# Kernel tuning notes

Hardware: AMD Instinct MI355X
Metric: run time of the kernel (lower is better)

The kernel has to match this reference:

```python
import jax, jax.numpy as jnp
import numpy as np

U, I, D, NNZ = 100000, 50000, 64, 6000000
N = U + I

def setup_inputs() -> dict:
    key = jax.random.key(0)
    ks = jax.random.split(key, 8)
    return {
        'user_emb': jax.random.normal(ks[0], (U, D), dtype=jnp.float32) * 0.1,
        'item_emb': jax.random.normal(ks[1], (I, D), dtype=jnp.float32) * 0.1,
        'adj_val': jax.random.uniform(ks[2], (NNZ,), dtype=jnp.float32) * 0.01,
        'adj_row': jax.random.randint(ks[3], (NNZ,), 0, N, dtype=jnp.int32),
        'adj_col': jax.random.randint(ks[4], (NNZ,), 0, N, dtype=jnp.int32),
        'users': jax.random.randint(ks[5], (4096,), 0, U, dtype=jnp.int32),
        'pos_items': jax.random.randint(ks[6], (4096,), 0, I, dtype=jnp.int32),
        'neg_items': jax.random.randint(ks[7], (4096,), 0, I, dtype=jnp.int32),
        'num_layers': 3,
    }

def spmm(val, row, col, x, n):
    # out[r] = sum_{e: row[e]==r} val[e] * x[col[e]]
    return jax.ops.segment_sum(val[:, None] * x[col], row, num_segments=n)

def reference(user_emb, item_emb, adj_val, adj_row, adj_col, users, pos_items, neg_items, num_layers):
    n = user_emb.shape[0] + item_emb.shape[0]
    ego = jnp.concatenate([user_emb, item_emb], axis=0)   # [N, D]
    acc = ego
    cur = ego
    for _ in range(num_layers):
        cur = spmm(adj_val, adj_row, adj_col, cur, n)
        acc = acc + cur
    final = acc / jnp.asarray(num_layers + 1, dtype=ego.dtype)  # mean over stacked layers
    u_g = final[:user_emb.shape[0]]
    i_g = final[user_emb.shape[0]:]
    return (u_g[users], i_g[pos_items], i_g[neg_items], u_g, i_g)
```

## Files before the change

kernel.cpp:

```cpp
#include <hip/hip_runtime.h>


#define U_CNT 100000
#define I_CNT 50000
#define N_CNT 150000
#define DIM 64
#define NNZ_CNT 6000000
#define NSEL 4096

#define NBKT 512
#define BROWS 293
#define BKT_OF(r) ((int)(((unsigned long long)(unsigned)(r) * 114521ull) >> 25))
#define BCAP 13312

#define BIN_BLK 512
#define BIN_THR 256

__device__ __forceinline__ unsigned short f32_to_bf16_rne(float f) {
    unsigned u = __float_as_uint(f);
    u += 0x7FFFu + ((u >> 16) & 1u);
    return (unsigned short)(u >> 16);
}
__device__ __forceinline__ float bf16_lo(unsigned u) {
    return __uint_as_float(u << 16);
}
__device__ __forceinline__ float bf16_hi(unsigned u) {
    return __uint_as_float(u & 0xFFFF0000u);
}


__global__ void init_kernel(const float* __restrict__ user_emb,
                            const float* __restrict__ item_emb,
                            unsigned short* __restrict__ cur,
                            float* __restrict__ acc) {
    const int total = N_CNT * DIM / 4;
    const int ubound = U_CNT * DIM / 4;
    const float4* ue = (const float4*)user_emb;
    const float4* ie = (const float4*)item_emb;
    float4* a4 = (float4*)acc;
    ushort4* c4 = (ushort4*)cur;
    for (int i = blockIdx.x * blockDim.x + threadIdx.x; i < total;
         i += gridDim.x * blockDim.x) {
        float4 v = (i < ubound) ? ue[i] : ie[i - ubound];
        ushort4 cv;
        cv.x = f32_to_bf16_rne(v.x);
        cv.y = f32_to_bf16_rne(v.y);
        cv.z = f32_to_bf16_rne(v.z);
        cv.w = f32_to_bf16_rne(v.w);
        c4[i] = cv;
        float4 a = v;
        a.x *= 0.25f; a.y *= 0.25f; a.z *= 0.25f; a.w *= 0.25f;
        a4[i] = a;
    }
}

__global__ void gather_kernel(const float* __restrict__ final_emb,
                              const int* __restrict__ users,
                              const int* __restrict__ pos,
                              const int* __restrict__ neg,
                              float* __restrict__ out) {
    const int total = 3 * NSEL * (DIM / 4);
    const float4* f4 = (const float4*)final_emb;
    float4* o4 = (float4*)out;
    for (int i = blockIdx.x * blockDim.x + threadIdx.x; i < total;
         i += gridDim.x * blockDim.x) {
        const int rowi = i / (DIM / 4);
        const int d4 = i % (DIM / 4);
        int src;
        if (rowi < NSEL) {
            src = users[rowi];
        } else if (rowi < 2 * NSEL) {
            src = U_CNT + pos[rowi - NSEL];
        } else {
            src = U_CNT + neg[rowi - 2 * NSEL];
        }
        o4[i] = f4[src * (DIM / 4) + d4];
    }
}

__global__ void bin_scatter_kernel(const float* __restrict__ val,
                                   const int* __restrict__ row,
                                   const int* __restrict__ col,
                                   int* __restrict__ gcnt,
                                   int2* __restrict__ etmp) {
    __shared__ int h[NBKT];
    __shared__ int curs[NBKT];
    for (int i = threadIdx.x; i < NBKT; i += BIN_THR) h[i] = 0;
    __syncthreads();
    const int tid = blockIdx.x * BIN_THR + threadIdx.x;
    const int4* r4 = (const int4*)row;
    const int4* c4 = (const int4*)col;
    const float4* v4 = (const float4*)val;
    for (int g = tid; g < NNZ_CNT / 4; g += BIN_BLK * BIN_THR) {
        const int4 r = r4[g];
        atomicAdd(&h[BKT_OF(r.x)], 1);
        atomicAdd(&h[BKT_OF(r.y)], 1);
        atomicAdd(&h[BKT_OF(r.z)], 1);
        atomicAdd(&h[BKT_OF(r.w)], 1);
    }
    __syncthreads();
    for (int i = threadIdx.x; i < NBKT; i += BIN_THR) {
        const int c = h[i];
        int base = 0;
        if (c > 0) base = atomicAdd(&gcnt[i], c);
        curs[i] = i * BCAP + base;
    }
    __syncthreads();
    for (int g = tid; g < NNZ_CNT / 4; g += BIN_BLK * BIN_THR) {
        const int4 r = r4[g];
        const int4 c = c4[g];
        const float4 v = v4[g];
        {
            const int bk = BKT_OF(r.x);
            const int p = atomicAdd(&curs[bk], 1);
            etmp[p] = make_int2(c.x | ((r.x - bk * BROWS) << 18),
                                __float_as_int(v.x));
        }
        {
            const int bk = BKT_OF(r.y);
            const int p = atomicAdd(&curs[bk], 1);
            etmp[p] = make_int2(c.y | ((r.y - bk * BROWS) << 18),
                                __float_as_int(v.y));
        }
        {
            const int bk = BKT_OF(r.z);
            const int p = atomicAdd(&curs[bk], 1);
            etmp[p] = make_int2(c.z | ((r.z - bk * BROWS) << 18),
                                __float_as_int(v.z));
        }
        {
            const int bk = BKT_OF(r.w);
            const int p = atomicAdd(&curs[bk], 1);
            etmp[p] = make_int2(c.w | ((r.w - bk * BROWS) << 18),
                                __float_as_int(v.w));
        }
    }
}

__global__ void scan_tot_kernel(const int* __restrict__ gcnt,
                                int* __restrict__ boff) {
    __shared__ int s[NBKT];
    const int k = threadIdx.x;
    const int v = gcnt[k];
    s[k] = v;
    __syncthreads();
    for (int d = 1; d < NBKT; d <<= 1) {
        int t = (k >= d) ? s[k - d] : 0;
        __syncthreads();
        s[k] += t;
        __syncthreads();
    }
    boff[k] = s[k] - v;
    if (k == NBKT - 1) boff[NBKT] = s[k];
}

__global__ __launch_bounds__(1024) void csr_sort_kernel(
        const int2* __restrict__ etmp,
        const int* __restrict__ gcnt,
        const int* __restrict__ boff,
        int2* __restrict__ edges,
        int* __restrict__ off) {
    __shared__ int cnt[BROWS];
    __shared__ int start[BROWS];
    __shared__ int sc[1024];
    const int bkt = blockIdx.x;
    const int n = gcnt[bkt];
    const int sbeg = bkt * BCAP;
    const int dbeg = boff[bkt];
    const int tid = threadIdx.x;

    for (int i = tid; i < BROWS; i += 1024) cnt[i] = 0;
    __syncthreads();
    for (int e = tid; e < n; e += 1024)
        atomicAdd(&cnt[((unsigned)etmp[sbeg + e].x) >> 18], 1);
    __syncthreads();
    {
        const int v = (tid < BROWS) ? cnt[tid] : 0;
        sc[tid] = v;
        __syncthreads();
        for (int d = 1; d < 1024; d <<= 1) {
            int t = (tid >= d) ? sc[tid - d] : 0;
            __syncthreads();
            sc[tid] += t;
            __syncthreads();
        }
        if (tid < BROWS) start[tid] = sc[tid] - v;
    }
    __syncthreads();
    const int base_row = bkt * BROWS;
    for (int i = tid; i < BROWS; i += 1024) {
        if (base_row + i < N_CNT) off[base_row + i] = dbeg + start[i];
        cnt[i] = start[i];
    }
    if (bkt == 0 && tid == 0) off[N_CNT] = NNZ_CNT;
    __syncthreads();
    for (int e = tid; e < n; e += 1024) {
        const int2 ed = etmp[sbeg + e];
        const int rl = ((unsigned)ed.x) >> 18;
        const int p = atomicAdd(&cnt[rl], 1);
        edges[dbeg + p] = make_int2(ed.x & 0x3FFFF, ed.y);
    }
}

__global__ void spmm_csr_kernel(const int2* __restrict__ edges,
                                const int* __restrict__ off,
                                const unsigned short* __restrict__ x,
                                unsigned short* __restrict__ y,
                                float* __restrict__ acc,
                                int write_y) {
    const int lane = threadIdx.x & 63;
    const int o = lane >> 3;
    const int t = lane & 7;
    const int gw = (blockIdx.x * blockDim.x + threadIdx.x) >> 6;
    const int totalWaves = (gridDim.x * blockDim.x) >> 6;
    const unsigned short* xt = x + (t << 3);
    for (int r = gw; r < N_CNT; r += totalWaves) {
        const int beg = off[r];
        const int end = off[r + 1];
        const int nfull = (end - beg) & ~15;
        const int mend = beg + nfull;
        float s0 = 0.f, s1 = 0.f, s2 = 0.f, s3 = 0.f;
        float s4 = 0.f, s5 = 0.f, s6 = 0.f, s7 = 0.f;
        #pragma unroll 2
        for (int e0 = beg; e0 < mend; e0 += 16) {
            const int2 eva = edges[e0 + o];
            const int2 evb = edges[e0 + o + 8];
            const float va = __int_as_float(eva.y);
            const float vb = __int_as_float(evb.y);
            const uint4 xa = *(const uint4*)(xt + ((size_t)(unsigned)eva.x << 6));
            const uint4 xb = *(const uint4*)(xt + ((size_t)(unsigned)evb.x << 6));
            s0 += va * bf16_lo(xa.x); s1 += va * bf16_hi(xa.x);
            s2 += va * bf16_lo(xa.y); s3 += va * bf16_hi(xa.y);
            s4 += va * bf16_lo(xa.z); s5 += va * bf16_hi(xa.z);
            s6 += va * bf16_lo(xa.w); s7 += va * bf16_hi(xa.w);
            s0 += vb * bf16_lo(xb.x); s1 += vb * bf16_hi(xb.x);
            s2 += vb * bf16_lo(xb.y); s3 += vb * bf16_hi(xb.y);
            s4 += vb * bf16_lo(xb.z); s5 += vb * bf16_hi(xb.z);
            s6 += vb * bf16_lo(xb.w); s7 += vb * bf16_hi(xb.w);
        }
        if (mend < end) {
            const int ea = mend + o;
            const int eb = ea + 8;
            int2 eva = make_int2(0, 0), evb = make_int2(0, 0);
            if (ea < end) eva = edges[ea];
            if (eb < end) evb = edges[eb];
            const float va = __int_as_float(eva.y);
            const float vb = __int_as_float(evb.y);
            const uint4 xa = *(const uint4*)(xt + ((size_t)(unsigned)eva.x << 6));
            const uint4 xb = *(const uint4*)(xt + ((size_t)(unsigned)evb.x << 6));
            s0 += va * bf16_lo(xa.x); s1 += va * bf16_hi(xa.x);
            s2 += va * bf16_lo(xa.y); s3 += va * bf16_hi(xa.y);
            s4 += va * bf16_lo(xa.z); s5 += va * bf16_hi(xa.z);
            s6 += va * bf16_lo(xa.w); s7 += va * bf16_hi(xa.w);
            s0 += vb * bf16_lo(xb.x); s1 += vb * bf16_hi(xb.x);
            s2 += vb * bf16_lo(xb.y); s3 += vb * bf16_hi(xb.y);
            s4 += vb * bf16_lo(xb.z); s5 += vb * bf16_hi(xb.z);
            s6 += vb * bf16_lo(xb.w); s7 += vb * bf16_hi(xb.w);
        }
        s0 += __shfl_xor(s0, 8); s0 += __shfl_xor(s0, 16); s0 += __shfl_xor(s0, 32);
        s1 += __shfl_xor(s1, 8); s1 += __shfl_xor(s1, 16); s1 += __shfl_xor(s1, 32);
        s2 += __shfl_xor(s2, 8); s2 += __shfl_xor(s2, 16); s2 += __shfl_xor(s2, 32);
        s3 += __shfl_xor(s3, 8); s3 += __shfl_xor(s3, 16); s3 += __shfl_xor(s3, 32);
        s4 += __shfl_xor(s4, 8); s4 += __shfl_xor(s4, 16); s4 += __shfl_xor(s4, 32);
        s5 += __shfl_xor(s5, 8); s5 += __shfl_xor(s5, 16); s5 += __shfl_xor(s5, 32);
        s6 += __shfl_xor(s6, 8); s6 += __shfl_xor(s6, 16); s6 += __shfl_xor(s6, 32);
        s7 += __shfl_xor(s7, 8); s7 += __shfl_xor(s7, 16); s7 += __shfl_xor(s7, 32);
        if (lane < 8) {
            if (write_y) {
                uint4 cv;
                cv.x = (unsigned)f32_to_bf16_rne(s0) |
                       ((unsigned)f32_to_bf16_rne(s1) << 16);
                cv.y = (unsigned)f32_to_bf16_rne(s2) |
                       ((unsigned)f32_to_bf16_rne(s3) << 16);
                cv.z = (unsigned)f32_to_bf16_rne(s4) |
                       ((unsigned)f32_to_bf16_rne(s5) << 16);
                cv.w = (unsigned)f32_to_bf16_rne(s6) |
                       ((unsigned)f32_to_bf16_rne(s7) << 16);
                ((uint4*)(y + ((size_t)r << 6)))[t] = cv;
            }
            float4* a4 = (float4*)(acc + ((size_t)r << 6) + (t << 3));
            float4 a0 = a4[0];
            float4 a1 = a4[1];
            a0.x += 0.25f * s0; a0.y += 0.25f * s1;
            a0.z += 0.25f * s2; a0.w += 0.25f * s3;
            a1.x += 0.25f * s4; a1.y += 0.25f * s5;
            a1.z += 0.25f * s6; a1.w += 0.25f * s7;
            a4[0] = a0;
            a4[1] = a1;
        }
    }
}


__global__ void init_f32_kernel(const float* __restrict__ user_emb,
                                const float* __restrict__ item_emb,
                                float* __restrict__ cur,
                                float* __restrict__ acc) {
    const int total = N_CNT * DIM / 4;
    const int ubound = U_CNT * DIM / 4;
    const float4* ue = (const float4*)user_emb;
    const float4* ie = (const float4*)item_emb;
    float4* c4 = (float4*)cur;
    float4* a4 = (float4*)acc;
    for (int i = blockIdx.x * blockDim.x + threadIdx.x; i < total;
         i += gridDim.x * blockDim.x) {
        float4 v = (i < ubound) ? ue[i] : ie[i - ubound];
        c4[i] = v;
        float4 a = v;
        a.x *= 0.25f; a.y *= 0.25f; a.z *= 0.25f; a.w *= 0.25f;
        a4[i] = a;
    }
}

__global__ void spmm_atomic_kernel(const float* __restrict__ val,
                                   const int* __restrict__ row,
                                   const int* __restrict__ col,
                                   const float* __restrict__ x,
                                   float* __restrict__ y) {
    const int lane = threadIdx.x & 63;
    const int gw = (blockIdx.x * blockDim.x + threadIdx.x) >> 6;
    const int totalWaves = (gridDim.x * blockDim.x) >> 6;
    for (int base = gw * 64; base < NNZ_CNT; base += totalWaves * 64) {
        const int e = base + lane;
        const float v = val[e];
        const int r = row[e];
        const int c = col[e];
        #pragma unroll 8
        for (int k = 0; k < 64; ++k) {
            const float vk = __shfl(v, k);
            const int rk = __shfl(r, k);
            const int ck = __shfl(c, k);
            atomicAdd(&y[rk * DIM + lane], vk * x[ck * DIM + lane]);
        }
    }
}

__global__ void accum_scale_kernel(float* __restrict__ acc,
                                   const float* __restrict__ nxt,
                                   float wacc) {
    const int total = N_CNT * DIM / 4;
    float4* a4 = (float4*)acc;
    const float4* n4 = (const float4*)nxt;
    for (int i = blockIdx.x * blockDim.x + threadIdx.x; i < total;
         i += gridDim.x * blockDim.x) {
        float4 a = a4[i];
        const float4 n = n4[i];
        a.x += wacc * n.x; a.y += wacc * n.y; a.z += wacc * n.z; a.w += wacc * n.w;
        a4[i] = a;
    }
}


extern "C" void kernel_launch(void* const* d_in, const int* in_sizes, int n_in,
                              void* d_out, int out_size, void* d_ws, size_t ws_size,
                              hipStream_t stream) {
    const float* user_emb  = (const float*)d_in[0];
    const float* item_emb  = (const float*)d_in[1];
    const float* adj_val   = (const float*)d_in[2];
    const int*   adj_row   = (const int*)d_in[3];
    const int*   adj_col   = (const int*)d_in[4];
    const int*   users     = (const int*)d_in[5];
    const int*   pos_items = (const int*)d_in[6];
    const int*   neg_items = (const int*)d_in[7];

    float* out       = (float*)d_out;
    float* out_sel   = out;
    float* final_emb = out + (size_t)3 * NSEL * DIM;
    float* acc       = final_emb;

    const size_t NBH = (size_t)N_CNT * DIM * 2;
    char* ws = (char*)d_ws;
    int2* etmp = (int2*)(ws + 0);
    unsigned short* bufA = (unsigned short*)(ws + 0);
    unsigned short* bufB = (unsigned short*)(ws + NBH);

    const size_t offE    = (size_t)NBKT * BCAP * 8;
    const size_t offG    = offE + (size_t)NNZ_CNT * 8;
    const size_t offBoff = offG + 4096;
    const size_t offOff  = offBoff + 4096;
    const size_t needed  = offOff + (size_t)(N_CNT + 1) * 4 + 64;

    if (ws_size >= needed) {
        int2* edges = (int2*)(ws + offE);
        int*  gcnt  = (int*)(ws + offG);
        int*  boff  = (int*)(ws + offBoff);
        int*  offp  = (int*)(ws + offOff);

        (void)hipMemsetAsync(gcnt, 0, NBKT * sizeof(int), stream);
        bin_scatter_kernel<<<BIN_BLK, BIN_THR, 0, stream>>>(adj_val, adj_row,
                                                            adj_col, gcnt,
                                                            etmp);
        scan_tot_kernel<<<1, NBKT, 0, stream>>>(gcnt, boff);
        csr_sort_kernel<<<NBKT, 1024, 0, stream>>>(etmp, gcnt, boff, edges,
                                                   offp);

        init_kernel<<<2048, 256, 0, stream>>>(user_emb, item_emb, bufA, acc);

        unsigned short* cur = bufA;
        unsigned short* nxt = bufB;
        for (int l = 0; l < 3; ++l) {
            spmm_csr_kernel<<<2048, 256, 0, stream>>>(edges, offp, cur, nxt, acc,
                                                      (l < 2) ? 1 : 0);
            unsigned short* t = cur; cur = nxt; nxt = t;
        }
    } else {
        float* fA = (float*)(ws + 0);
        float* fB = (float*)(ws + (size_t)N_CNT * DIM * sizeof(float));
        init_f32_kernel<<<2048, 256, 0, stream>>>(user_emb, item_emb, fA, acc);
        float* cur = fA;
        float* nxt = fB;
        for (int l = 0; l < 3; ++l) {
            (void)hipMemsetAsync(nxt, 0, (size_t)N_CNT * DIM * sizeof(float),
                                 stream);
            spmm_atomic_kernel<<<2048, 256, 0, stream>>>(adj_val, adj_row,
                                                         adj_col, cur, nxt);
            accum_scale_kernel<<<2048, 256, 0, stream>>>(acc, nxt, 0.25f);
            float* t = cur; cur = nxt; nxt = t;
        }
    }

    gather_kernel<<<768, 256, 0, stream>>>(final_emb, users, pos_items,
                                           neg_items, out_sel);
}
```

Baseline: 466.5 us.

## Fuse bucket-offset scan into CSR sort and interleave two rows per wave in SpMM

Measured after the change: 562.1 us. +20.5%, slower.

```diff
diff --git a/kernel.cpp b/kernel.cpp
--- a/kernel.cpp
+++ b/kernel.cpp
@@ -78,6 +78,7 @@
     }
 }
 
+
 __global__ void bin_scatter_kernel(const float* __restrict__ val,
                                    const int* __restrict__ row,
                                    const int* __restrict__ col,
@@ -137,42 +138,39 @@
     }
 }
 
-__global__ void scan_tot_kernel(const int* __restrict__ gcnt,
-                                int* __restrict__ boff) {
-    __shared__ int s[NBKT];
-    const int k = threadIdx.x;
-    const int v = gcnt[k];
-    s[k] = v;
-    __syncthreads();
-    for (int d = 1; d < NBKT; d <<= 1) {
-        int t = (k >= d) ? s[k - d] : 0;
-        __syncthreads();
-        s[k] += t;
-        __syncthreads();
-    }
-    boff[k] = s[k] - v;
-    if (k == NBKT - 1) boff[NBKT] = s[k];
-}
-
 __global__ __launch_bounds__(1024) void csr_sort_kernel(
         const int2* __restrict__ etmp,
         const int* __restrict__ gcnt,
-        const int* __restrict__ boff,
         int2* __restrict__ edges,
         int* __restrict__ off) {
     __shared__ int cnt[BROWS];
     __shared__ int start[BROWS];
     __shared__ int sc[1024];
     const int bkt = blockIdx.x;
+    const int tid = threadIdx.x;
     const int n = gcnt[bkt];
     const int sbeg = bkt * BCAP;
-    const int dbeg = boff[bkt];
-    const int tid = threadIdx.x;
+
+    sc[tid] = (tid < bkt) ? gcnt[tid] : 0;
+    __syncthreads();
+    for (int d = 512; d >= 1; d >>= 1) {
+        if (tid < d) sc[tid] += sc[tid + d];
+        __syncthreads();
+    }
+    const int dbeg = sc[0];
+    __syncthreads();
 
     for (int i = tid; i < BROWS; i += 1024) cnt[i] = 0;
     __syncthreads();
-    for (int e = tid; e < n; e += 1024)
-        atomicAdd(&cnt[((unsigned)etmp[sbeg + e].x) >> 18], 1);
+    const int npair = n >> 1;
+    const int4* et4 = (const int4*)(etmp + sbeg);
+    for (int p = tid; p < npair; p += 1024) {
+        const int4 ed = et4[p];
+        atomicAdd(&cnt[((unsigned)ed.x) >> 18], 1);
+        atomicAdd(&cnt[((unsigned)ed.z) >> 18], 1);
+    }
+    if (tid == 0 && (n & 1))
+        atomicAdd(&cnt[((unsigned)etmp[sbeg + n - 1].x) >> 18], 1);
     __syncthreads();
     {
         const int v = (tid < BROWS) ? cnt[tid] : 0;
@@ -194,11 +192,100 @@
     }
     if (bkt == 0 && tid == 0) off[N_CNT] = NNZ_CNT;
     __syncthreads();
-    for (int e = tid; e < n; e += 1024) {
-        const int2 ed = etmp[sbeg + e];
+    for (int p = tid; p < npair; p += 1024) {
+        const int4 ed = et4[p];
+        int rl = ((unsigned)ed.x) >> 18;
+        int q = atomicAdd(&cnt[rl], 1);
+        edges[dbeg + q] = make_int2(ed.x & 0x3FFFF, ed.y);
+        rl = ((unsigned)ed.z) >> 18;
+        q = atomicAdd(&cnt[rl], 1);
+        edges[dbeg + q] = make_int2(ed.z & 0x3FFFF, ed.w);
+    }
+    if (tid == 0 && (n & 1)) {
+        const int2 ed = etmp[sbeg + n - 1];
         const int rl = ((unsigned)ed.x) >> 18;
-        const int p = atomicAdd(&cnt[rl], 1);
-        edges[dbeg + p] = make_int2(ed.x & 0x3FFFF, ed.y);
+        const int q = atomicAdd(&cnt[rl], 1);
+        edges[dbeg + q] = make_int2(ed.x & 0x3FFFF, ed.y);
+    }
+}
+
+
+__device__ __forceinline__ void block16(const int2* __restrict__ edges,
+                                        int e0, int o,
+                                        const unsigned short* __restrict__ xt,
+                                        float (&s)[8]) {
+    const int2 eva = edges[e0 + o];
+    const int2 evb = edges[e0 + o + 8];
+    const float va = __int_as_float(eva.y);
+    const float vb = __int_as_float(evb.y);
+    const uint4 xa = *(const uint4*)(xt + ((size_t)(unsigned)eva.x << 6));
+    const uint4 xb = *(const uint4*)(xt + ((size_t)(unsigned)evb.x << 6));
+    s[0] += va * bf16_lo(xa.x); s[1] += va * bf16_hi(xa.x);
+    s[2] += va * bf16_lo(xa.y); s[3] += va * bf16_hi(xa.y);
+    s[4] += va * bf16_lo(xa.z); s[5] += va * bf16_hi(xa.z);
+    s[6] += va * bf16_lo(xa.w); s[7] += va * bf16_hi(xa.w);
+    s[0] += vb * bf16_lo(xb.x); s[1] += vb * bf16_hi(xb.x);
+    s[2] += vb * bf16_lo(xb.y); s[3] += vb * bf16_hi(xb.y);
+    s[4] += vb * bf16_lo(xb.z); s[5] += vb * bf16_hi(xb.z);
+    s[6] += vb * bf16_lo(xb.w); s[7] += vb * bf16_hi(xb.w);
+}
+
+__device__ __forceinline__ void tail16(const int2* __restrict__ edges,
+                                       int mend, int end, int o,
+                                       const unsigned short* __restrict__ xt,
+                                       float (&s)[8]) {
+    const int ea = mend + o;
+    const int eb = ea + 8;
+    int2 eva = make_int2(0, 0), evb = make_int2(0, 0);
+    if (ea < end) eva = edges[ea];
+    if (eb < end) evb = edges[eb];
+    const float va = __int_as_float(eva.y);
+    const float vb = __int_as_float(evb.y);
+    const uint4 xa = *(const uint4*)(xt + ((size_t)(unsigned)eva.x << 6));
+    const uint4 xb = *(const uint4*)(xt + ((size_t)(unsigned)evb.x << 6));
+    s[0] += va * bf16_lo(xa.x); s[1] += va * bf16_hi(xa.x);
+    s[2] += va * bf16_lo(xa.y); s[3] += va * bf16_hi(xa.y);
+    s[4] += va * bf16_lo(xa.z); s[5] += va * bf16_hi(xa.z);
+    s[6] += va * bf16_lo(xa.w); s[7] += va * bf16_hi(xa.w);
+    s[0] += vb * bf16_lo(xb.x); s[1] += vb * bf16_hi(xb.x);
+    s[2] += vb * bf16_lo(xb.y); s[3] += vb * bf16_hi(xb.y);
+    s[4] += vb * bf16_lo(xb.z); s[5] += vb * bf16_hi(xb.z);
+    s[6] += vb * bf16_lo(xb.w); s[7] += vb * bf16_hi(xb.w);
+}
+
+__device__ __forceinline__ void reduce_write(float (&s)[8], int r, int lane,
+                                             int t,
+                                             unsigned short* __restrict__ y,
+                                             float* __restrict__ acc,
+                                             int write_y) {
+    #pragma unroll
+    for (int i = 0; i < 8; ++i) {
+        s[i] += __shfl_xor(s[i], 8);
+        s[i] += __shfl_xor(s[i], 16);
+        s[i] += __shfl_xor(s[i], 32);
+    }
+    if (lane < 8) {
+        if (write_y) {
+            uint4 cv;
+            cv.x = (unsigned)f32_to_bf16_rne(s[0]) |
+                   ((unsigned)f32_to_bf16_rne(s[1]) << 16);
+            cv.y = (unsigned)f32_to_bf16_rne(s[2]) |
+                   ((unsigned)f32_to_bf16_rne(s[3]) << 16);
+            cv.z = (unsigned)f32_to_bf16_rne(s[4]) |
+                   ((unsigned)f32_to_bf16_rne(s[5]) << 16);
+            cv.w = (unsigned)f32_to_bf16_rne(s[6]) |
+                   ((unsigned)f32_to_bf16_rne(s[7]) << 16);
+            ((uint4*)(y + ((size_t)r << 6)))[t] = cv;
+        }
+        float4* a4 = (float4*)(acc + ((size_t)r << 6) + (t << 3));
+        float4 a0 = a4[0];
+        float4 a1 = a4[1];
+        a0.x += 0.25f * s[0]; a0.y += 0.25f * s[1];
+        a0.z += 0.25f * s[2]; a0.w += 0.25f * s[3];
+        a1.x += 0.25f * s[4]; a1.y += 0.25f * s[5];
+        a1.z += 0.25f * s[6]; a1.w += 0.25f * s[7];
+        a4[0] = a0;
+        a4[1] = a1;
     }
 }
 
@@ -214,80 +301,30 @@
     const int gw = (blockIdx.x * blockDim.x + threadIdx.x) >> 6;
     const int totalWaves = (gridDim.x * blockDim.x) >> 6;
     const unsigned short* xt = x + (t << 3);
-    for (int r = gw; r < N_CNT; r += totalWaves) {
-        const int beg = off[r];
-        const int end = off[r + 1];
-        const int nfull = (end - beg) & ~15;
-        const int mend = beg + nfull;
-        float s0 = 0.f, s1 = 0.f, s2 = 0.f, s3 = 0.f;
-        float s4 = 0.f, s5 = 0.f, s6 = 0.f, s7 = 0.f;
+    for (int r0 = gw; r0 < N_CNT; r0 += 2 * totalWaves) {
+        const int r1 = r0 + totalWaves;
+        const int begA = off[r0];
+        const int endA = off[r0 + 1];
+        int begB = 0, endB = 0;
+        if (r1 < N_CNT) { begB = off[r1]; endB = off[r1 + 1]; }
+        const int mendA = begA + ((endA - begA) & ~15);
+        const int mendB = begB + ((endB - begB) & ~15);
+        float sA[8] = {0.f, 0.f, 0.f, 0.f, 0.f, 0.f, 0.f, 0.f};
+        float sB[8] = {0.f, 0.f, 0.f, 0.f, 0.f, 0.f, 0.f, 0.f};
+        int eA = begA, eB = begB;
+        while (eA < mendA && eB < mendB) {
+            block16(edges, eA, o, xt, sA);
+            block16(edges, eB, o, xt, sB);
+            eA += 16; eB += 16;
+        }
         #pragma unroll 2
-        for (int e0 = beg; e0 < mend; e0 += 16) {
-            const int2 eva = edges[e0 + o];
-            const int2 evb = edges[e0 + o + 8];
-            const float va = __int_as_float(eva.y);
-            const float vb = __int_as_float(evb.y);
-            const uint4 xa = *(const uint4*)(xt + ((size_t)(unsigned)eva.x << 6));
-            const uint4 xb = *(const uint4*)(xt + ((size_t)(unsigned)evb.x << 6));
-            s0 += va * bf16_lo(xa.x); s1 += va * bf16_hi(xa.x);
-            s2 += va * bf16_lo(xa.y); s3 += va * bf16_hi(xa.y);
-            s4 += va * bf16_lo(xa.z); s5 += va * bf16_hi(xa.z);
-            s6 += va * bf16_lo(xa.w); s7 += va * bf16_hi(xa.w);
-            s0 += vb * bf16_lo(xb.x); s1 += vb * bf16_hi(xb.x);
-            s2 += vb * bf16_lo(xb.y); s3 += vb * bf16_hi(xb.y);
-            s4 += vb * bf16_lo(xb.z); s5 += vb * bf16_hi(xb.z);
-            s6 += vb * bf16_lo(xb.w); s7 += vb * bf16_hi(xb.w);
-        }
-        if (mend < end) {
-            const int ea = mend + o;
-            const int eb = ea + 8;
-            int2 eva = make_int2(0, 0), evb = make_int2(0, 0);
-            if (ea < end) eva = edges[ea];
-            if (eb < end) evb = edges[eb];
-            const float va = __int_as_float(eva.y);
-            const float vb = __int_as_float(evb.y);
-            const uint4 xa = *(const uint4*)(xt + ((size_t)(unsigned)eva.x << 6));
-            const uint4 xb = *(const uint4*)(xt + ((size_t)(unsigned)evb.x << 6));
-            s0 += va * bf16_lo(xa.x); s1 += va * bf16_hi(xa.x);
-            s2 += va * bf16_lo(xa.y); s3 += va * bf16_hi(xa.y);
-            s4 += va * bf16_lo(xa.z); s5 += va * bf16_hi(xa.z);
-            s6 += va * bf16_lo(xa.w); s7 += va * bf16_hi(xa.w);
-            s0 += vb * bf16_lo(xb.x); s1 += vb * bf16_hi(xb.x);
-            s2 += vb * bf16_lo(xb.y); s3 += vb * bf16_hi(xb.y);
-            s4 += vb * bf16_lo(xb.z); s5 += vb * bf16_hi(xb.z);
-            s6 += vb * bf16_lo(xb.w); s7 += vb * bf16_hi(xb.w);
-        }
-        s0 += __shfl_xor(s0, 8); s0 += __shfl_xor(s0, 16); s0 += __shfl_xor(s0, 32);
-        s1 += __shfl_xor(s1, 8); s1 += __shfl_xor(s1, 16); s1 += __shfl_xor(s1, 32);
-        s2 += __shfl_xor(s2, 8); s2 += __shfl_xor(s2, 16); s2 += __shfl_xor(s2, 32);
-        s3 += __shfl_xor(s3, 8); s3 += __shfl_xor(s3, 16); s3 += __shfl_xor(s3, 32);
-        s4 += __shfl_xor(s4, 8); s4 += __shfl_xor(s4, 16); s4 += __shfl_xor(s4, 32);
-        s5 += __shfl_xor(s5, 8); s5 += __shfl_xor(s5, 16); s5 += __shfl_xor(s5, 32);
-        s6 += __shfl_xor(s6, 8); s6 += __shfl_xor(s6, 16); s6 += __shfl_xor(s6, 32);
-        s7 += __shfl_xor(s7, 8); s7 += __shfl_xor(s7, 16); s7 += __shfl_xor(s7, 32);
-        if (lane < 8) {
-            if (write_y) {
-                uint4 cv;
-                cv.x = (unsigned)f32_to_bf16_rne(s0) |
-                       ((unsigned)f32_to_bf16_rne(s1) << 16);
-                cv.y = (unsigned)f32_to_bf16_rne(s2) |
-                       ((unsigned)f32_to_bf16_rne(s3) << 16);
-                cv.z = (unsigned)f32_to_bf16_rne(s4) |
-                       ((unsigned)f32_to_bf16_rne(s5) << 16);
-                cv.w = (unsigned)f32_to_bf16_rne(s6) |
-                       ((unsigned)f32_to_bf16_rne(s7) << 16);
-                ((uint4*)(y + ((size_t)r << 6)))[t] = cv;
-            }
-            float4* a4 = (float4*)(acc + ((size_t)r << 6) + (t << 3));
-            float4 a0 = a4[0];
-            float4 a1 = a4[1];
-            a0.x += 0.25f * s0; a0.y += 0.25f * s1;
-            a0.z += 0.25f * s2; a0.w += 0.25f * s3;
-            a1.x += 0.25f * s4; a1.y += 0.25f * s5;
-            a1.z += 0.25f * s6; a1.w += 0.25f * s7;
-            a4[0] = a0;
-            a4[1] = a1;
-        }
+        for (; eA < mendA; eA += 16) block16(edges, eA, o, xt, sA);
+        #pragma unroll 2
+        for (; eB < mendB; eB += 16) block16(edges, eB, o, xt, sB);
+        if (eA < endA) tail16(edges, eA, endA, o, xt, sA);
+        if (eB < endB) tail16(edges, eB, endB, o, xt, sB);
+        reduce_write(sA, r0, lane, t, y, acc, write_y);
+        if (r1 < N_CNT) reduce_write(sB, r1, lane, t, y, acc, write_y);
     }
 }
 
@@ -376,23 +413,19 @@
 
     const size_t offE    = (size_t)NBKT * BCAP * 8;
     const size_t offG    = offE + (size_t)NNZ_CNT * 8;
-    const size_t offBoff = offG + 4096;
-    const size_t offOff  = offBoff + 4096;
+    const size_t offOff  = offG + 4096;
     const size_t needed  = offOff + (size_t)(N_CNT + 1) * 4 + 64;
 
     if (ws_size >= needed) {
         int2* edges = (int2*)(ws + offE);
         int*  gcnt  = (int*)(ws + offG);
-        int*  boff  = (int*)(ws + offBoff);
         int*  offp  = (int*)(ws + offOff);
 
         (void)hipMemsetAsync(gcnt, 0, NBKT * sizeof(int), stream);
         bin_scatter_kernel<<<BIN_BLK, BIN_THR, 0, stream>>>(adj_val, adj_row,
                                                             adj_col, gcnt,
                                                             etmp);
-        scan_tot_kernel<<<1, NBKT, 0, stream>>>(gcnt, boff);
-        csr_sort_kernel<<<NBKT, 1024, 0, stream>>>(etmp, gcnt, boff, edges,
-                                                   offp);
+        csr_sort_kernel<<<NBKT, 1024, 0, stream>>>(etmp, gcnt, edges, offp);
 
         init_kernel<<<2048, 256, 0, stream>>>(user_emb, item_emb, bufA, acc);
 
```
